# Performance work log

Measured on AMD Instinct MI355X. Metric: run time of the kernel, lower is better.

The kernel has to match this reference:

```python
import jax, jax.numpy as jnp
import numpy as np
import math

B, S, D, H = 2, 2048, 1024, 16
DK = D // H


def setup_inputs() -> dict:
    key = jax.random.key(0)
    k1, k2, k3, k4, k5, k6 = jax.random.split(key, 6)
    scale = 1.0 / math.sqrt(D)
    return {
        "query": jax.random.normal(k1, (B, S, D), dtype=jnp.float32),
        "key": jax.random.normal(k2, (B, S, D), dtype=jnp.float32),
        "value": jax.random.normal(k3, (B, S, D), dtype=jnp.float32),
        "Wqkv": jax.random.normal(k4, (D, D), dtype=jnp.float32) * scale,
        "Wout": jax.random.normal(k5, (D, D), dtype=jnp.float32) * scale,
        "mask": jax.random.randint(k6, (B, 1, S, S), 0, 2, dtype=jnp.int32),
    }


def reference(query, key, value, Wqkv, Wout, mask):
    # Single shared QKV projection (same weight applied to q, k, v), no bias.
    q = query @ Wqkv.T
    k = key @ Wqkv.T
    v = value @ Wqkv.T
    # Faithful to the original: reshape (B, S, D) -> (B, H, S, DK) directly
    # (torch .reshape(n_batches, h, -1, d_k), NOT view+transpose).
    q = q.reshape(B, H, S, DK)
    k = k.reshape(B, H, S, DK)
    v = v.reshape(B, H, S, DK)
    scores = jnp.einsum("bhqd,bhkd->bhqk", q, k) / math.sqrt(DK)
    scores = jnp.where(mask == 0, jnp.float32(-1e9), scores)
    p_attn = jax.nn.softmax(scores, axis=-1)  # dropout is identity in eval
    x = jnp.einsum("bhqk,bhkd->bhqd", p_attn, v)  # [B,H,S,DK]
    x = x.transpose(0, 2, 1, 3).reshape(B, S, H * DK)
    return x @ Wout.T
```

## Files before the change

kernel.cpp:

```cpp
#include <hip/hip_runtime.h>
#include <stdint.h>


typedef __bf16 bf16;
typedef __bf16 bf16x8 __attribute__((ext_vector_type(8)));
typedef __bf16 bf16x4 __attribute__((ext_vector_type(4)));
typedef float f32x4 __attribute__((ext_vector_type(4)));

#define MFMA16(a, b, c) __builtin_amdgcn_mfma_f32_16x16x32_bf16((a), (b), (c), 0, 0, 0)
#define EXP2(x) __builtin_amdgcn_exp2f(x)

static constexpr int BATCH = 2;
static constexpr int SEQ = 2048;
static constexpr int DIM = 1024;
static constexpr int DK = 64;
static constexpr float QSCALE = 0.125f * 1.44269504088896340736f;

template <typename T>
struct Stripe;
template <>
struct Stripe<bf16> {
  uint4 v;
};
template <>
struct Stripe<float> {
  float4 a, b;
};

__device__ inline Stripe<bf16> load_stripe(const bf16* p) {
  Stripe<bf16> s;
  s.v = *(const uint4*)p;
  return s;
}
__device__ inline Stripe<float> load_stripe(const float* p) {
  Stripe<float> s;
  s.a = *(const float4*)p;
  s.b = *(const float4*)(p + 4);
  return s;
}
__device__ inline void store_stripe(bf16* d, const Stripe<bf16>& s) { *(uint4*)d = s.v; }
__device__ inline void store_stripe(bf16* d, const Stripe<float>& s) {
  bf16x8 v;
  v[0] = (bf16)s.a.x;
  v[1] = (bf16)s.a.y;
  v[2] = (bf16)s.a.z;
  v[3] = (bf16)s.a.w;
  v[4] = (bf16)s.b.x;
  v[5] = (bf16)s.b.y;
  v[6] = (bf16)s.b.z;
  v[7] = (bf16)s.b.w;
  *(bf16x8*)d = v;
}

__global__ __launch_bounds__(256) void mask_bits_kernel(const int* __restrict__ mask,
                                                        unsigned long long* __restrict__ bits) {
  int idx = blockIdx.x * 256 + threadIdx.x;
  int m = mask[idx];
  unsigned long long bal = __ballot(m != 0);
  if ((threadIdx.x & 63) == 0) bits[idx >> 6] = bal;
}

template <int BM, typename TA, typename TW, typename TC>
__global__ __launch_bounds__(256, 2) void gemm_bt(const TA* __restrict__ A0,
                                                  const TA* __restrict__ A1,
                                                  const TA* __restrict__ A2,
                                                  const TW* __restrict__ W,
                                                  TC* __restrict__ C0,
                                                  TC* __restrict__ C1,
                                                  TC* __restrict__ C2,
                                                  float scale0) {
  constexpr int K = 1024, N = 1024, LDA = 40;
  constexpr int MT = BM / 32;
  __shared__ bf16 As[BM * LDA];
  __shared__ bf16 Bs[128 * LDA];

  const TA* A = (blockIdx.z == 0) ? A0 : (blockIdx.z == 1) ? A1 : A2;
  TC* C = (blockIdx.z == 0) ? C0 : (blockIdx.z == 1) ? C1 : C2;
  const float sc = (blockIdx.z == 0) ? scale0 : 1.0f;

  const int tid = threadIdx.x;
  const int lane = tid & 63;
  const int wv = tid >> 6;
  const int wm = wv >> 1, wn = wv & 1;
  const int lrow = lane & 15, quad = lane >> 4;
  const int m0 = blockIdx.y * BM, n0 = blockIdx.x * 128;

  const f32x4 fz = {0.f, 0.f, 0.f, 0.f};
  f32x4 acc[MT][4];
#pragma unroll
  for (int i = 0; i < MT; ++i)
#pragma unroll
    for (int j = 0; j < 4; ++j) acc[i][j] = fz;

  const int r0 = tid >> 2;
  const int c0 = (tid & 3) * 8;
  const TA* pa0 = A + (size_t)(m0 + r0) * K + c0;
  const TA* pa1 = A + (size_t)(m0 + (r0 & (BM - 1) | 64 & (BM - 1)) ) * K + c0;
  const TW* pb0 = W + (size_t)(n0 + r0) * K + c0;
  const TW* pb1 = W + (size_t)(n0 + r0 + 64) * K + c0;
  bf16* wa0 = &As[r0 * LDA + c0];
  bf16* wa1 = &As[((r0 + 64) & (BM * 2 - 1)) * LDA + c0];
  bf16* wb0 = &Bs[r0 * LDA + c0];
  bf16* wb1 = &Bs[(r0 + 64) * LDA + c0];
  if constexpr (BM == 128) pa1 = A + (size_t)(m0 + r0 + 64) * K + c0;

  Stripe<TA> ra0 = load_stripe(pa0);
  Stripe<TA> ra1;
  if constexpr (BM == 128) ra1 = load_stripe(pa1);
  Stripe<TW> rb0 = load_stripe(pb0);
  Stripe<TW> rb1 = load_stripe(pb1);

  for (int k0 = 0; k0 < K; k0 += 32) {
    __syncthreads();
    store_stripe(wa0, ra0);
    if constexpr (BM == 128) store_stripe(wa1, ra1);
    store_stripe(wb0, rb0);
    store_stripe(wb1, rb1);
    __syncthreads();
    if (k0 + 32 < K) {
      ra0 = load_stripe(pa0 + k0 + 32);
      if constexpr (BM == 128) ra1 = load_stripe(pa1 + k0 + 32);
      rb0 = load_stripe(pb0 + k0 + 32);
      rb1 = load_stripe(pb1 + k0 + 32);
    }
    bf16x8 af[MT], bfr[4];
#pragma unroll
    for (int mt = 0; mt < MT; ++mt)
      af[mt] = *(const bf16x8*)(&As[(wm * (BM / 2) + mt * 16 + lrow) * LDA + quad * 8]);
#pragma unroll
    for (int nt = 0; nt < 4; ++nt)
      bfr[nt] = *(const bf16x8*)(&Bs[(wn * 64 + nt * 16 + lrow) * LDA + quad * 8]);
#pragma unroll
    for (int mt = 0; mt < MT; ++mt)
#pragma unroll
      for (int nt = 0; nt < 4; ++nt) acc[mt][nt] = MFMA16(af[mt], bfr[nt], acc[mt][nt]);
  }

#pragma unroll
  for (int mt = 0; mt < MT; ++mt) {
    const int gm = m0 + wm * (BM / 2) + mt * 16 + quad * 4;
#pragma unroll
    for (int nt = 0; nt < 4; ++nt) {
      const int gn = n0 + wn * 64 + nt * 16 + lrow;
#pragma unroll
      for (int r = 0; r < 4; ++r) C[(size_t)(gm + r) * N + gn] = (TC)(acc[mt][nt][r] * sc);
    }
  }
}

__global__ __launch_bounds__(256, 2) void attn_kernel(const bf16* __restrict__ Qg,
                                                      const bf16* __restrict__ Kg,
                                                      const bf16* __restrict__ Vg,
                                                      const unsigned* __restrict__ bits,
                                                      bf16* __restrict__ Y) {
  constexpr int LQ = 72;
  __shared__ bf16 Qs[128 * LQ];
  __shared__ bf16 Ks[64 * LQ];
  __shared__ bf16 Vts[64 * LQ];
  __shared__ bf16 Ps[4][32 * LQ];

  const int tid = threadIdx.x;
  const int lane = tid & 63;
  const int wv = tid >> 6;
  const int lrow = lane & 15, quad = lane >> 4;
  const int bh = blockIdx.y;
  const int b = bh >> 4, h = bh & 15;
  const int q0 = blockIdx.x * 128;

  const bf16* Qh = Qg + (size_t)bh * (SEQ * DK);
  const bf16* Kh = Kg + (size_t)bh * (SEQ * DK);
  const bf16* Vh = Vg + (size_t)bh * (SEQ * DK);

#pragma unroll
  for (int i = 0; i < 4; ++i) {
    int s = tid + i * 256;
    int row = s >> 3, c8 = (s & 7) * 8;
    *(uint4*)(&Qs[row * LQ + c8]) = *(const uint4*)(Qh + (size_t)(q0 + row) * DK + c8);
  }

  const int krow = tid >> 3;
  const int kc8 = (tid & 7) * 8;
  const bf16* pk0 = Kh + (size_t)krow * DK + kc8;
  const bf16* pk1 = Kh + (size_t)(krow + 32) * DK + kc8;
  const int vn2 = tid & 31;
  const int vk2b = tid >> 5;
  const bf16* pv0 = Vh + (size_t)(vk2b + 0) * 2 * DK + vn2 * 2;
  const bf16* pv1 = Vh + (size_t)(vk2b + 8) * 2 * DK + vn2 * 2;
  const bf16* pv2 = Vh + (size_t)(vk2b + 16) * 2 * DK + vn2 * 2;
  const bf16* pv3 = Vh + (size_t)(vk2b + 24) * 2 * DK + vn2 * 2;

  uint4 kr0, kr1;
  uint32_t va[4], vb[4];

  kr0 = *(const uint4*)(pk0);
  kr1 = *(const uint4*)(pk1);
  va[0] = *(const uint32_t*)(pv0);
  vb[0] = *(const uint32_t*)(pv0 + DK);
  va[1] = *(const uint32_t*)(pv1);
  vb[1] = *(const uint32_t*)(pv1 + DK);
  va[2] = *(const uint32_t*)(pv2);
  vb[2] = *(const uint32_t*)(pv2 + DK);
  va[3] = *(const uint32_t*)(pv3);
  vb[3] = *(const uint32_t*)(pv3 + DK);
  *(uint4*)(&Ks[krow * LQ + kc8]) = kr0;
  *(uint4*)(&Ks[(krow + 32) * LQ + kc8]) = kr1;
#pragma unroll
  for (int i = 0; i < 4; ++i) {
    uint32_t t0 = (va[i] & 0xffffu) | (vb[i] << 16);
    uint32_t t1 = (va[i] >> 16) | (vb[i] & 0xffff0000u);
    *(uint32_t*)(&Vts[(vn2 * 2) * LQ + (vk2b + i * 8) * 2]) = t0;
    *(uint32_t*)(&Vts[(vn2 * 2 + 1) * LQ + (vk2b + i * 8) * 2]) = t1;
  }
  __syncthreads();

  bf16x8 qf[2][2];
#pragma unroll
  for (int nt = 0; nt < 2; ++nt)
#pragma unroll
    for (int ks = 0; ks < 2; ++ks)
      qf[nt][ks] = *(const bf16x8*)(&Qs[(wv * 32 + nt * 16 + lrow) * LQ + ks * 32 + quad * 8]);
  __syncthreads();

  const f32x4 fz = {0.f, 0.f, 0.f, 0.f};
  f32x4 of_t[4][2];
#pragma unroll
  for (int i = 0; i < 4; ++i)
#pragma unroll
    for (int j = 0; j < 2; ++j) of_t[i][j] = fz;
  float lsum[2] = {0.f, 0.f};

  const unsigned* bitrow = bits + (size_t)b * SEQ * (SEQ / 32);

  for (int kt = 0; kt < 32; ++kt) {
    const int cur = kt & 1;
    bf16* kb = cur ? Qs : Ks;
    bf16* vbuf = cur ? (Qs + 64 * LQ) : Vts;
    if (kt + 1 < 32) {
      const size_t adv = (size_t)(kt + 1) * 64 * DK;
      kr0 = *(const uint4*)(pk0 + adv);
      kr1 = *(const uint4*)(pk1 + adv);
      va[0] = *(const uint32_t*)(pv0 + adv);
      vb[0] = *(const uint32_t*)(pv0 + adv + DK);
      va[1] = *(const uint32_t*)(pv1 + adv);
      vb[1] = *(const uint32_t*)(pv1 + adv + DK);
      va[2] = *(const uint32_t*)(pv2 + adv);
      vb[2] = *(const uint32_t*)(pv2 + adv + DK);
      va[3] = *(const uint32_t*)(pv3 + adv);
      vb[3] = *(const uint32_t*)(pv3 + adv + DK);
    }
    uint2 mwn[2];
#pragma unroll
    for (int nt = 0; nt < 2; ++nt) {
      int row = q0 + wv * 32 + nt * 16 + lrow;
      mwn[nt] = *(const uint2*)(bitrow + (size_t)row * (SEQ / 32) + kt * 2);
    }

    f32x4 st[4][2];
#pragma unroll
    for (int mt = 0; mt < 4; ++mt)
#pragma unroll
      for (int nt = 0; nt < 2; ++nt) st[mt][nt] = fz;
#pragma unroll
    for (int ks = 0; ks < 2; ++ks) {
#pragma unroll
      for (int mt = 0; mt < 4; ++mt) {
        bf16x8 kfv = *(const bf16x8*)(kb + (mt * 16 + lrow) * LQ + ks * 32 + quad * 8);
#pragma unroll
        for (int nt = 0; nt < 2; ++nt) st[mt][nt] = MFMA16(kfv, qf[nt][ks], st[mt][nt]);
      }
    }

#pragma unroll
    for (int nt = 0; nt < 2; ++nt) {
      uint32_t ux = mwn[nt].x >> (quad * 4);
      uint32_t uy = mwn[nt].y >> (quad * 4);
      float psum = 0.f;
#pragma unroll
      for (int mt = 0; mt < 4; ++mt) {
        uint32_t u = (mt & 2) ? uy : ux;
        int sh = (mt & 1) << 4;
        bf16x4 pk;
#pragma unroll
        for (int r = 0; r < 4; ++r) {
          float p = EXP2(st[mt][nt][r]);
          p = ((u >> (sh + r)) & 1u) ? p : 0.f;
          psum += p;
          pk[r] = (bf16)p;
        }
        *(bf16x4*)(&Ps[wv][(nt * 16 + lrow) * LQ + mt * 16 + quad * 4]) = pk;
      }
      lsum[nt] += psum;
    }

#pragma unroll
    for (int ks = 0; ks < 2; ++ks) {
      bf16x8 avf[4], bpf[2];
#pragma unroll
      for (int dkt = 0; dkt < 4; ++dkt)
        avf[dkt] = *(const bf16x8*)(vbuf + (dkt * 16 + lrow) * LQ + ks * 32 + quad * 8);
#pragma unroll
      for (int rt = 0; rt < 2; ++rt)
        bpf[rt] = *(const bf16x8*)(&Ps[wv][(rt * 16 + lrow) * LQ + ks * 32 + quad * 8]);
#pragma unroll
      for (int dkt = 0; dkt < 4; ++dkt)
#pragma unroll
        for (int rt = 0; rt < 2; ++rt) of_t[dkt][rt] = MFMA16(avf[dkt], bpf[rt], of_t[dkt][rt]);
    }

    if (kt + 1 < 32) {
      bf16* kbn = cur ? Ks : Qs;
      bf16* vbn = cur ? Vts : (Qs + 64 * LQ);
      *(uint4*)(kbn + krow * LQ + kc8) = kr0;
      *(uint4*)(kbn + (krow + 32) * LQ + kc8) = kr1;
#pragma unroll
      for (int i = 0; i < 4; ++i) {
        uint32_t t0 = (va[i] & 0xffffu) | (vb[i] << 16);
        uint32_t t1 = (va[i] >> 16) | (vb[i] & 0xffff0000u);
        *(uint32_t*)(vbn + (vn2 * 2) * LQ + (vk2b + i * 8) * 2) = t0;
        *(uint32_t*)(vbn + (vn2 * 2 + 1) * LQ + (vk2b + i * 8) * 2) = t1;
      }
    }
    __syncthreads();
  }

  float linv[2];
#pragma unroll
  for (int nt = 0; nt < 2; ++nt) {
    float v = lsum[nt];
    v += __shfl_xor(v, 16);
    v += __shfl_xor(v, 32);
    linv[nt] = 1.0f / fmaxf(v, 1e-20f);
  }

#pragma unroll
  for (int dkt = 0; dkt < 4; ++dkt)
#pragma unroll
    for (int rt = 0; rt < 2; ++rt) {
      bf16x4 o;
#pragma unroll
      for (int j = 0; j < 4; ++j) o[j] = (bf16)(of_t[dkt][rt][j] * linv[rt]);
      const int row = q0 + wv * 32 + rt * 16 + lrow;
      *(bf16x4*)(&Y[((size_t)b * SEQ + row) * DIM + h * 64 + dkt * 16 + quad * 4]) = o;
    }
}

extern "C" void kernel_launch(void* const* d_in, const int* in_sizes, int n_in,
                              void* d_out, int out_size, void* d_ws, size_t ws_size,
                              hipStream_t stream) {
  const float* query = (const float*)d_in[0];
  const float* key = (const float*)d_in[1];
  const float* value = (const float*)d_in[2];
  const float* Wqkv = (const float*)d_in[3];
  const float* Wout = (const float*)d_in[4];
  const int* mask = (const int*)d_in[5];
  float* out = (float*)d_out;

  char* ws = (char*)d_ws;
  bf16* q = (bf16*)(ws);
  bf16* k = (bf16*)(ws + 8388608);
  bf16* v = (bf16*)(ws + 16777216);
  bf16* y = (bf16*)(ws + 25165824);
  unsigned long long* bits64 = (unsigned long long*)(ws + 33554432);

  mask_bits_kernel<<<(BATCH * SEQ * SEQ) / 256, 256, 0, stream>>>(mask, bits64);

  gemm_bt<128, float, float, bf16>
      <<<dim3(8, 32, 3), 256, 0, stream>>>(query, key, value, Wqkv, q, k, v, QSCALE);

  attn_kernel<<<dim3(16, 32), 256, 0, stream>>>(q, k, v, (const unsigned*)bits64, y);

  gemm_bt<64, bf16, float, float>
      <<<dim3(8, 64, 1), 256, 0, stream>>>(y, y, y, Wout, out, out, out, 1.0f);
}
```

Measured before the change: 283.4 us.

## Pre-convert inputs to bf16 and use direct global-to-LDS loads in GEMMs

Adds a conversion kernel that casts the fp32 activations and weights to bf16 in workspace. It also adds a new GEMM that stages tiles with global_load_lds (direct global-to-LDS DMA) over a 64-wide K step, replacing the register-staged, fp32-converting GEMM. The aim is to halve the GEMM's global read traffic and remove the register round-trip. The cost is extra conversion passes and more workspace, and the new GEMM has no double buffering. A fallback keeps the old path when the workspace is too small.

```diff
diff --git a/kernel.cpp b/kernel.cpp
--- a/kernel.cpp
+++ b/kernel.cpp
@@ -15,6 +15,11 @@
 static constexpr int DIM = 1024;
 static constexpr int DK = 64;
 static constexpr float QSCALE = 0.125f * 1.44269504088896340736f;
+
+__device__ __forceinline__ void gld16(const bf16* g, bf16* l) {
+  __builtin_amdgcn_global_load_lds((const __attribute__((address_space(1))) void*)g,
+                                   (__attribute__((address_space(3))) void*)l, 16, 0, 0);
+}
 
 template <typename T>
 struct Stripe;
@@ -52,12 +57,110 @@
   *(bf16x8*)d = v;
 }
 
+__global__ __launch_bounds__(256) void conv3_kernel(const float* __restrict__ x0,
+                                                    const float* __restrict__ x1,
+                                                    const float* __restrict__ x2,
+                                                    bf16* __restrict__ d0,
+                                                    bf16* __restrict__ d1,
+                                                    bf16* __restrict__ d2) {
+  const float* x = (blockIdx.y == 0) ? x0 : (blockIdx.y == 1) ? x1 : x2;
+  bf16* d = (blockIdx.y == 0) ? d0 : (blockIdx.y == 1) ? d1 : d2;
+  size_t i = ((size_t)blockIdx.x * 256 + threadIdx.x) * 8;
+  float4 a = *(const float4*)(x + i);
+  float4 b = *(const float4*)(x + i + 4);
+  bf16x8 v;
+  v[0] = (bf16)a.x;
+  v[1] = (bf16)a.y;
+  v[2] = (bf16)a.z;
+  v[3] = (bf16)a.w;
+  v[4] = (bf16)b.x;
+  v[5] = (bf16)b.y;
+  v[6] = (bf16)b.z;
+  v[7] = (bf16)b.w;
+  *(bf16x8*)(d + i) = v;
+}
+
 __global__ __launch_bounds__(256) void mask_bits_kernel(const int* __restrict__ mask,
                                                         unsigned long long* __restrict__ bits) {
   int idx = blockIdx.x * 256 + threadIdx.x;
   int m = mask[idx];
   unsigned long long bal = __ballot(m != 0);
   if ((threadIdx.x & 63) == 0) bits[idx >> 6] = bal;
+}
+
+template <typename TC>
+__global__ __launch_bounds__(256) void gemm_lds(const bf16* __restrict__ A0,
+                                                const bf16* __restrict__ A1,
+                                                const bf16* __restrict__ A2,
+                                                const bf16* __restrict__ W,
+                                                TC* __restrict__ C0,
+                                                TC* __restrict__ C1,
+                                                TC* __restrict__ C2,
+                                                float scale0) {
+  constexpr int K = 1024, N = 1024;
+  __shared__ bf16 As[128 * 64];
+  __shared__ bf16 Bs[128 * 64];
+
+  const bf16* A = (blockIdx.z == 0) ? A0 : (blockIdx.z == 1) ? A1 : A2;
+  TC* C = (blockIdx.z == 0) ? C0 : (blockIdx.z == 1) ? C1 : C2;
+  const float sc = (blockIdx.z == 0) ? scale0 : 1.0f;
+
+  const int tid = threadIdx.x;
+  const int lane = tid & 63;
+  const int wv = tid >> 6;
+  const int wm = wv >> 1, wn = wv & 1;
+  const int lrow = lane & 15, quad = lane >> 4;
+  const int m0 = blockIdx.y * 128, n0 = blockIdx.x * 128;
+
+  const int srow = tid & 127;
+  const int hi = tid >> 7;
+  const bf16* ga = A + (size_t)(m0 + srow) * K;
+  const bf16* gb = W + (size_t)(n0 + srow) * K;
+
+  const f32x4 fz = {0.f, 0.f, 0.f, 0.f};
+  f32x4 acc[4][4];
+#pragma unroll
+  for (int i = 0; i < 4; ++i)
+#pragma unroll
+    for (int j = 0; j < 4; ++j) acc[i][j] = fz;
+
+  for (int k0 = 0; k0 < K; k0 += 64) {
+    __syncthreads();
+#pragma unroll
+    for (int j = 0; j < 4; ++j) {
+      const int panel = j * 2 + hi;
+      const int soff = (j * 256 + tid) * 8;
+      gld16(ga + k0 + panel * 8, &As[soff]);
+      gld16(gb + k0 + panel * 8, &Bs[soff]);
+    }
+    __syncthreads();
+
+#pragma unroll
+    for (int ks = 0; ks < 2; ++ks) {
+      bf16x8 af[4], bfm[4];
+#pragma unroll
+      for (int mt = 0; mt < 4; ++mt)
+        af[mt] = *(const bf16x8*)(&As[(ks * 4 + quad) * 1024 + (wm * 64 + mt * 16 + lrow) * 8]);
+#pragma unroll
+      for (int nt = 0; nt < 4; ++nt)
+        bfm[nt] = *(const bf16x8*)(&Bs[(ks * 4 + quad) * 1024 + (wn * 64 + nt * 16 + lrow) * 8]);
+#pragma unroll
+      for (int mt = 0; mt < 4; ++mt)
+#pragma unroll
+        for (int nt = 0; nt < 4; ++nt) acc[mt][nt] = MFMA16(af[mt], bfm[nt], acc[mt][nt]);
+    }
+  }
+
+#pragma unroll
+  for (int mt = 0; mt < 4; ++mt) {
+    const int gm = m0 + wm * 64 + mt * 16 + quad * 4;
+#pragma unroll
+    for (int nt = 0; nt < 4; ++nt) {
+      const int gn = n0 + wn * 64 + nt * 16 + lrow;
+#pragma unroll
+      for (int r = 0; r < 4; ++r) C[(size_t)(gm + r) * N + gn] = (TC)(acc[mt][nt][r] * sc);
+    }
+  }
 }
 
 template <int BM, typename TA, typename TW, typename TC>
@@ -95,11 +198,11 @@
   const int r0 = tid >> 2;
   const int c0 = (tid & 3) * 8;
   const TA* pa0 = A + (size_t)(m0 + r0) * K + c0;
-  const TA* pa1 = A + (size_t)(m0 + (r0 & (BM - 1) | 64 & (BM - 1)) ) * K + c0;
+  const TA* pa1 = pa0;
   const TW* pb0 = W + (size_t)(n0 + r0) * K + c0;
   const TW* pb1 = W + (size_t)(n0 + r0 + 64) * K + c0;
   bf16* wa0 = &As[r0 * LDA + c0];
-  bf16* wa1 = &As[((r0 + 64) & (BM * 2 - 1)) * LDA + c0];
+  bf16* wa1 = &As[((r0 + 64) & (2 * BM - 1)) * LDA + c0];
   bf16* wb0 = &Bs[r0 * LDA + c0];
   bf16* wb1 = &Bs[(r0 + 64) * LDA + c0];
   if constexpr (BM == 128) pa1 = A + (size_t)(m0 + r0 + 64) * K + c0;
@@ -356,19 +459,35 @@
   float* out = (float*)d_out;
 
   char* ws = (char*)d_ws;
+  constexpr size_t MB = 1048576;
   bf16* q = (bf16*)(ws);
-  bf16* k = (bf16*)(ws + 8388608);
-  bf16* v = (bf16*)(ws + 16777216);
-  bf16* y = (bf16*)(ws + 25165824);
-  unsigned long long* bits64 = (unsigned long long*)(ws + 33554432);
+  bf16* k = (bf16*)(ws + 8 * MB);
+  bf16* v = (bf16*)(ws + 16 * MB);
+  bf16* y = (bf16*)(ws + 24 * MB);
+  unsigned long long* bits64 = (unsigned long long*)(ws + 32 * MB);
 
   mask_bits_kernel<<<(BATCH * SEQ * SEQ) / 256, 256, 0, stream>>>(mask, bits64);
 
-  gemm_bt<128, float, float, bf16>
-      <<<dim3(8, 32, 3), 256, 0, stream>>>(query, key, value, Wqkv, q, k, v, QSCALE);
-
-  attn_kernel<<<dim3(16, 32), 256, 0, stream>>>(q, k, v, (const unsigned*)bits64, y);
-
-  gemm_bt<64, bf16, float, float>
-      <<<dim3(8, 64, 1), 256, 0, stream>>>(y, y, y, Wout, out, out, out, 1.0f);
-}
+  if (ws_size >= 61 * MB) {
+    bf16* qb = (bf16*)(ws + 33 * MB);
+    bf16* kb = (bf16*)(ws + 41 * MB);
+    bf16* vb = (bf16*)(ws + 49 * MB);
+    bf16* Wqb = (bf16*)(ws + 57 * MB);
+    bf16* Wob = (bf16*)(ws + 59 * MB);
+
+    conv3_kernel<<<dim3(2048, 3), 256, 0, stream>>>(query, key, value, qb, kb, vb);
+    conv3_kernel<<<dim3(512, 2), 256, 0, stream>>>(Wqkv, Wout, Wout, Wqb, Wob, Wob);
+
+    gemm_lds<bf16><<<dim3(8, 32, 3), 256, 0, stream>>>(qb, kb, vb, Wqb, q, k, v, QSCALE);
+
+    attn_kernel<<<dim3(16, 32), 256, 0, stream>>>(q, k, v, (const unsigned*)bits64, y);
+
+    gemm_lds<float><<<dim3(8, 32, 1), 256, 0, stream>>>(y, y, y, Wob, out, out, out, 1.0f);
+  } else {
+    gemm_bt<128, float, float, bf16>
+        <<<dim3(8, 32, 3), 256, 0, stream>>>(query, key, value, Wqkv, q, k, v, QSCALE);
+    attn_kernel<<<dim3(16, 32), 256, 0, stream>>>(q, k, v, (const unsigned*)bits64, y);
+    gemm_bt<64, bf16, float, float>
+        <<<dim3(8, 64, 1), 256, 0, stream>>>(y, y, y, Wout, out, out, out, 1.0f);
+  }
+}
```

Result: slower. 304.3 us (+7.4%).
